# Kernel optimization log

Hardware: AMD Instinct MI355X
Metric: run time of the kernel (lower is better)

## Reference

```python
import jax, jax.numpy as jnp
import numpy as np


def conv2d(x, w, b, pad):
    # x: [B,Cin,H,W], w: [Cout,Cin,kh,kw]
    y = jax.lax.conv_general_dilated(
        x, w, window_strides=(1, 1), padding=[(pad, pad), (pad, pad)],
        dimension_numbers=('NCHW', 'OIHW', 'NCHW'))
    return y + b[None, :, None, None]


def setup_inputs() -> dict:
    key = jax.random.key(0)
    ks = jax.random.split(key, 11)
    B, C, H, W = 4, 128, 64, 64
    Cc, Hc, Wc = 256, 32, 32
    s = 0.05
    return {
        'sr_feat': jax.random.normal(ks[0], (B, C, H, W), jnp.float32),
        'context_feat': jax.random.normal(ks[1], (B, Cc, Hc, Wc), jnp.float32),
        'Wq': jax.random.normal(ks[2], (C, C, 1, 1), jnp.float32) * s,
        'bq': jax.random.normal(ks[3], (C,), jnp.float32) * s,
        'Wk': jax.random.normal(ks[4], (C, Cc, 1, 1), jnp.float32) * s,
        'bk': jax.random.normal(ks[5], (C,), jnp.float32) * s,
        'Wv': jax.random.normal(ks[6], (C, Cc, 1, 1), jnp.float32) * s,
        'bv': jax.random.normal(ks[7], (C,), jnp.float32) * s,
        'Wp': jax.random.normal(ks[8], (C, C, 3, 3), jnp.float32) * s,
        'bp': jax.random.normal(ks[9], (C,), jnp.float32) * s,
        'gamma': jax.random.normal(ks[10], (1,), jnp.float32) * s,
    }


def reference(sr_feat, context_feat, Wq, bq, Wk, bk, Wv, bv, Wp, bp, gamma):
    B, C, H, W = sr_feat.shape
    Cc = context_feat.shape[1]
    # bilinear upsample (half-pixel centers == align_corners=False)
    ctx = jax.image.resize(context_feat, (B, Cc, H, W), method='bilinear')
    q = conv2d(sr_feat, Wq, bq, 0).reshape(B, C, H * W)   # [B,C,N]
    k = conv2d(ctx, Wk, bk, 0).reshape(B, C, H * W)       # [B,C,N]
    v = conv2d(ctx, Wv, bv, 0).reshape(B, C, H * W)       # [B,C,N]
    # attn[b,n,m] = softmax_m( sum_c q[b,c,n] * k[b,c,m] )
    attn = jax.nn.softmax(jnp.einsum('bcn,bcm->bnm', q, k), axis=-1)
    # out[b,c,n] = sum_m v[b,c,m] * attn[b,n,m]
    out = jnp.einsum('bcm,bnm->bcn', v, attn).reshape(B, C, H, W)
    return sr_feat + gamma[0] * conv2d(out, Wp, bp, 1)
```

## Files before the change

### kernel.cpp

```cpp
#include <hip/hip_runtime.h>
#include <math.h>

#define NB 4
#define C  128
#define CCH 256
#define HH 64
#define WW 64
#define NN 4096
#define HC 32
#define WC 32
#define PP 66
#define LOG2E 1.44269504088896f
#define NSPLIT 4

typedef unsigned short u16;
typedef unsigned int uint32;
typedef short s16x8 __attribute__((ext_vector_type(8)));
typedef float f32x4 __attribute__((ext_vector_type(4)));
typedef float f32x16 __attribute__((ext_vector_type(16)));

__device__ __forceinline__ u16 f2bf(float f) {
    uint32 u = __float_as_uint(f);
    u += 0x7fffu + ((u >> 16) & 1u);
    return (u16)(u >> 16);
}
__device__ __forceinline__ float bf2f(u16 h) {
    return __uint_as_float((uint32)h << 16);
}

__global__ __launch_bounds__(256) void prep_all(const float* __restrict__ ctx,
                                                const float* __restrict__ sr,
                                                const float* __restrict__ Wq,
                                                const float* __restrict__ Wk,
                                                const float* __restrict__ Wv,
                                                const float* __restrict__ Wp,
                                                u16* __restrict__ ctx_t,
                                                u16* __restrict__ sr_t,
                                                u16* __restrict__ wbf,
                                                u16* __restrict__ wt,
                                                uint4* __restrict__ att_z) {
    __shared__ float smem[2 * 32 * 130];
    int blk = blockIdx.x;
    int tid = threadIdx.x;

    if (blk < 512) {
        float (*ls)[32][130] = (float(*)[32][130])smem;
        int y = blk & 63;
        int cch = (blk >> 6) & 1;
        int b = blk >> 7;
        float sy = y * 0.5f - 0.25f;
        int y0 = (int)floorf(sy);
        float wy = sy - (float)y0;
        int y0c = y0 < 0 ? 0 : y0;
        int y1c = (y0 + 1 > HC - 1) ? HC - 1 : y0 + 1;
#pragma unroll
        for (int t = 0; t < 4; t++) {
            int CI = t * 256 + tid;
            int cc = CI >> 3, xq = CI & 7;
            const float* s = ctx + (size_t)(b * CCH + cch * 128 + cc) * (HC * WC);
            float4 v0 = *(const float4*)(s + y0c * WC + xq * 4);
            float4 v1 = *(const float4*)(s + y1c * WC + xq * 4);
            ls[0][xq * 4 + 0][cc] = v0.x; ls[0][xq * 4 + 1][cc] = v0.y;
            ls[0][xq * 4 + 2][cc] = v0.z; ls[0][xq * 4 + 3][cc] = v0.w;
            ls[1][xq * 4 + 0][cc] = v1.x; ls[1][xq * 4 + 1][cc] = v1.y;
            ls[1][xq * 4 + 2][cc] = v1.z; ls[1][xq * 4 + 3][cc] = v1.w;
        }
        __syncthreads();
        int occ = tid & 127, xh = tid >> 7;
        u16* ob = ctx_t + ((size_t)b * NN + (size_t)y * 64) * CCH + cch * 128 + occ;
        float wy1 = 1.f - wy;
#pragma unroll
        for (int xi = 0; xi < 32; xi++) {
            int x = xi * 2 + xh;
            float sx = x * 0.5f - 0.25f;
            int x0 = (int)floorf(sx);
            float wx = sx - (float)x0;
            int x0c = x0 < 0 ? 0 : x0;
            int x1c = (x0 + 1 > WC - 1) ? WC - 1 : x0 + 1;
            float v00 = ls[0][x0c][occ], v01 = ls[0][x1c][occ];
            float v10 = ls[1][x0c][occ], v11 = ls[1][x1c][occ];
            float val = wy1 * ((1.f - wx) * v00 + wx * v01)
                      + wy  * ((1.f - wx) * v10 + wx * v11);
            ob[(size_t)x * CCH] = f2bf(val);
        }
    } else if (blk < 1024) {
        float* ls = smem;
        int idx = blk - 512;
        int n0 = (idx & 63) * 64;
        int ci0 = ((idx >> 6) & 1) * 64;
        int b = idx >> 7;
        const float* inb = sr + ((size_t)b * C + ci0) * NN + n0;
#pragma unroll
        for (int L = 0; L < 4; L++) {
            int fc = tid + L * 256;
            int nc = fc & 15, ci = fc >> 4;
            float4 v = *(const float4*)(inb + (size_t)ci * NN + nc * 4);
            float* d = &ls[ci * 65 + nc * 4];
            d[0] = v.x; d[1] = v.y; d[2] = v.z; d[3] = v.w;
        }
        __syncthreads();
        u16* ob = sr_t + ((size_t)b * NN + n0) * C + ci0;
#pragma unroll
        for (int j = 0; j < 16; j++) {
            int o = tid + j * 256;
            int ci = o & 63, n = o >> 6;
            ob[(size_t)n * C + ci] = f2bf(ls[ci * 65 + n]);
        }
    } else if (blk < 1920) {
        int i = (blk - 1024) * 256 + tid;
        if (i < 81920) {
            float v;
            if (i < 16384) v = Wq[i] * LOG2E;
            else if (i < 49152) v = Wk[i - 16384];
            else v = Wv[i - 49152];
            wbf[i] = f2bf(v);
        } else {
            int idx = i - 81920;
            int ciin = idx & 31;
            int co = (idx >> 5) & 127;
            int cb = (idx >> 12) & 3;
            int pos = idx >> 14;
            int ky = pos / 3, kx = pos - ky * 3;
            int ci = cb * 32 + ciin;
            wt[idx] = f2bf(Wp[((size_t)(co * C + ci) * 3 + ky) * 3 + kx]);
        }
    } else {
        int i = (blk - 1920) * 256 + tid;
        if (i < 278784) att_z[i] = make_uint4(0, 0, 0, 0);
    }
}

__global__ __launch_bounds__(256) void proj_all(const u16* __restrict__ sr_t,
                                                const u16* __restrict__ ctx_t,
                                                const u16* __restrict__ wbf,
                                                const float* __restrict__ bq,
                                                const float* __restrict__ bk,
                                                const float* __restrict__ bv,
                                                u16* __restrict__ q_t,
                                                u16* __restrict__ k_t,
                                                u16* __restrict__ v_bf) {
    __shared__ u16 xs[128 * 64];
    __shared__ u16 wsm[128 * 64];
    int z = blockIdx.z;
    int b = blockIdx.y;
    int n0 = blockIdx.x * 128;
    int Cin = (z == 0) ? C : CCH;
    const u16* xb = (z == 0 ? sr_t : ctx_t) + (size_t)b * NN * Cin;
    const u16* wb = wbf + (z == 0 ? 0 : (z == 1 ? 16384 : 49152));
    const float* bias = (z == 0) ? bq : (z == 1 ? bk : bv);
    float bsc = (z == 0) ? LOG2E : 1.0f;
    bool vmode = (z == 2);

    int tid = threadIdx.x;
    int w = tid >> 6, lane = tid & 63, l31 = lane & 31, half = lane >> 5;
    int xh = w >> 1, wh = w & 1;

    f32x16 acc[2][2];
#pragma unroll
    for (int xt = 0; xt < 2; xt++)
#pragma unroll
        for (int wt2 = 0; wt2 < 2; wt2++)
#pragma unroll
            for (int i = 0; i < 16; i++) acc[xt][wt2][i] = 0.f;

    int nchunks = Cin >> 6;
    for (int c0i = 0; c0i < nchunks; c0i++) {
        int c0 = c0i * 64;
        __syncthreads();
#pragma unroll
        for (int t = 0; t < 4; t++) {
            int CI = t * 256 + tid;
            int row = CI >> 3, sl = CI & 7;
            int lc = sl ^ (row & 7);
            __builtin_amdgcn_global_load_lds(
                (const __attribute__((address_space(1))) void*)(xb + (size_t)(n0 + row) * Cin + c0 + lc * 8),
                (__attribute__((address_space(3))) void*)&xs[(size_t)CI * 8], 16, 0, 0);
        }
#pragma unroll
        for (int t = 0; t < 4; t++) {
            int CI = t * 256 + tid;
            int co = CI >> 3, sl = CI & 7;
            int lc = sl ^ (co & 7);
            __builtin_amdgcn_global_load_lds(
                (const __attribute__((address_space(1))) void*)(wb + (size_t)co * Cin + c0 + lc * 8),
                (__attribute__((address_space(3))) void*)&wsm[(size_t)CI * 8], 16, 0, 0);
        }
        __syncthreads();
#pragma unroll
        for (int kg = 0; kg < 4; kg++) {
            int pc = ((kg * 2 + half) ^ (l31 & 7)) * 8;
            s16x8 xf[2], wf2[2];
#pragma unroll
            for (int xt = 0; xt < 2; xt++)
                xf[xt] = *(const s16x8*)&xs[(xh * 64 + xt * 32 + l31) * 64 + pc];
#pragma unroll
            for (int wt2 = 0; wt2 < 2; wt2++)
                wf2[wt2] = *(const s16x8*)&wsm[(wh * 64 + wt2 * 32 + l31) * 64 + pc];
#pragma unroll
            for (int xt = 0; xt < 2; xt++)
#pragma unroll
                for (int wt2 = 0; wt2 < 2; wt2++) {
                    if (vmode)
                        acc[xt][wt2] = __builtin_amdgcn_mfma_f32_32x32x16_bf16(wf2[wt2], xf[xt], acc[xt][wt2], 0, 0, 0);
                    else
                        acc[xt][wt2] = __builtin_amdgcn_mfma_f32_32x32x16_bf16(xf[xt], wf2[wt2], acc[xt][wt2], 0, 0, 0);
                }
        }
    }

    if (!vmode) {
        u16* ot = (z == 0 ? q_t : k_t) + (size_t)b * NN * C;
        float bv2[2];
#pragma unroll
        for (int wt2 = 0; wt2 < 2; wt2++) bv2[wt2] = bias[wh * 64 + wt2 * 32 + l31] * bsc;
#pragma unroll
        for (int xt = 0; xt < 2; xt++)
#pragma unroll
            for (int r = 0; r < 16; r++) {
                int n = n0 + xh * 64 + xt * 32 + (r & 3) + 8 * (r >> 2) + 4 * half;
#pragma unroll
                for (int wt2 = 0; wt2 < 2; wt2++)
                    ot[(size_t)n * C + wh * 64 + wt2 * 32 + l31] = f2bf(acc[xt][wt2][r] + bv2[wt2]);
            }
    } else {
        u16* ov = v_bf + (size_t)b * C * NN;
#pragma unroll
        for (int wt2 = 0; wt2 < 2; wt2++)
#pragma unroll
            for (int r = 0; r < 16; r++) {
                int co = wh * 64 + wt2 * 32 + (r & 3) + 8 * (r >> 2) + 4 * half;
                float bvv = bias[co];
#pragma unroll
                for (int xt = 0; xt < 2; xt++) {
                    int n = n0 + xh * 64 + xt * 32 + l31;
                    ov[(size_t)co * NN + n] = f2bf(acc[xt][wt2][r] + bvv);
                }
            }
    }
}

__global__ __launch_bounds__(256) void flash_mfma(const u16* __restrict__ qt_p,
                                                  const u16* __restrict__ kt_p,
                                                  const u16* __restrict__ vt_p,
                                                  u16* __restrict__ part,
                                                  float* __restrict__ lpart) {
    __shared__ u16 ks[64 * 128];
    __shared__ u16 vs[128 * 64];

    int ib = blockIdx.x;
    int b = (ib & 7) >> 1;
    int rest = ((ib >> 3) << 1) | (ib & 1);
    int qtile = rest >> 2;
    int split = rest & 3;
    int n0 = qtile * 128;
    int tid = threadIdx.x;
    int w = tid >> 6, lane = tid & 63, l31 = lane & 31, half = lane >> 5;

    const u16* qtb = qt_p + (size_t)b * NN * C;
    const u16* ktb = kt_p + (size_t)b * NN * C;
    const u16* vtb = vt_p + (size_t)b * C * NN;

    auto stageK = [&](int m0) {
#pragma unroll
        for (int t = 0; t < 4; t++) {
            int CI = (w * 4 + t) * 64 + lane;
            int r = CI >> 4;
            int lc = (CI & 15) ^ (r & 15);
            __builtin_amdgcn_global_load_lds(
                (const __attribute__((address_space(1))) void*)(ktb + (size_t)(m0 + r) * C + lc * 8),
                (__attribute__((address_space(3))) void*)&ks[(w * 4 + t) * 512], 16, 0, 0);
        }
    };
    auto stageV = [&](int m0) {
#pragma unroll
        for (int t = 0; t < 4; t++) {
            int CI = (w * 4 + t) * 64 + lane;
            int c = CI >> 3;
            int lc = (CI & 7) ^ (c & 7);
            __builtin_amdgcn_global_load_lds(
                (const __attribute__((address_space(1))) void*)(vtb + (size_t)c * NN + m0 + lc * 8),
                (__attribute__((address_space(3))) void*)&vs[(w * 4 + t) * 512], 16, 0, 0);
        }
    };

    int qrow = n0 + w * 32 + l31;
    s16x8 qf[8];
#pragma unroll
    for (int kg = 0; kg < 8; kg++)
        qf[kg] = *(const s16x8*)(qtb + (size_t)qrow * C + kg * 16 + half * 8);

    int m_base = split * 1024;
    stageK(m_base);
    __syncthreads();

    f32x16 oacc[4];
#pragma unroll
    for (int mt = 0; mt < 4; mt++)
#pragma unroll
        for (int i = 0; i < 16; i++) oacc[mt][i] = 0.f;
    float lsum = 0.f;

    for (int it = 0; it < 16; it++) {
        int m0 = m_base + it * 64;
        stageV(m0);

        f32x16 st[2];
#pragma unroll
        for (int kmt = 0; kmt < 2; kmt++)
#pragma unroll
            for (int i = 0; i < 16; i++) st[kmt][i] = 0.f;
#pragma unroll
        for (int kg = 0; kg < 8; kg++) {
            int pc = ((kg * 2 + half) ^ (l31 & 15)) * 8;
#pragma unroll
            for (int kmt = 0; kmt < 2; kmt++) {
                s16x8 kf = *(const s16x8*)&ks[(kmt * 32 + l31) * 128 + pc];
                st[kmt] = __builtin_amdgcn_mfma_f32_32x32x16_bf16(kf, qf[kg], st[kmt], 0, 0, 0);
            }
        }
        __syncthreads();
        if (it < 15) stageK(m0 + 64);

#pragma unroll
        for (int kmt = 0; kmt < 2; kmt++) {
            float e[16];
            float ls = 0.f;
#pragma unroll
            for (int r = 0; r < 16; r++) { e[r] = exp2f(st[kmt][r]); ls += e[r]; }
            lsum += ls;
            uint32 A[4], B4[4];
#pragma unroll
            for (int g = 0; g < 4; g++) {
                A[g]  = __builtin_amdgcn_perm(__float_as_uint(e[4 * g + 1]), __float_as_uint(e[4 * g + 0]), 0x07060302u);
                B4[g] = __builtin_amdgcn_perm(__float_as_uint(e[4 * g + 3]), __float_as_uint(e[4 * g + 2]), 0x07060302u);
            }
#pragma unroll
            for (int s = 0; s < 2; s++) {
                uint32 sendA = half ? A[2 * s] : A[2 * s + 1];
                uint32 sendB = half ? B4[2 * s] : B4[2 * s + 1];
                uint32 rA = __shfl_xor(sendA, 32);
                uint32 rB = __shfl_xor(sendB, 32);
                uint32 oA = half ? A[2 * s + 1] : A[2 * s];
                uint32 oB = half ? B4[2 * s + 1] : B4[2 * s];
                union { uint32 u[4]; s16x8 v; } pu;
                pu.u[0] = half ? rA : oA;
                pu.u[1] = half ? rB : oB;
                pu.u[2] = half ? oA : rA;
                pu.u[3] = half ? oB : rB;
                s16x8 pf = pu.v;
                int kgp = kmt * 2 + s;
                int pcv = ((kgp * 2 + half) ^ (l31 & 7)) * 8;
#pragma unroll
                for (int mt = 0; mt < 4; mt++) {
                    s16x8 vf = *(const s16x8*)&vs[(mt * 32 + l31) * 64 + pcv];
                    oacc[mt] = __builtin_amdgcn_mfma_f32_32x32x16_bf16(vf, pf, oacc[mt], 0, 0, 0);
                }
            }
        }
        __syncthreads();
    }

    float lt = lsum + __shfl_xor(lsum, 32);
    if (half == 0) lpart[(size_t)split * NB * NN + (size_t)b * NN + qrow] = lt;
    u16* pb = part + ((size_t)split * NB + b) * (size_t)C * NN;
#pragma unroll
    for (int mt = 0; mt < 4; mt++)
#pragma unroll
        for (int r = 0; r < 16; r++) {
            int c = mt * 32 + (r & 3) + 8 * (r >> 2) + 4 * half;
            pb[(size_t)c * NN + n0 + w * 32 + l31] = f2bf(oacc[mt][r]);
        }
}

__global__ __launch_bounds__(256) void flash_combine(const u16* __restrict__ part,
                                                     const float* __restrict__ lpart,
                                                     u16* __restrict__ att_t) {
    __shared__ u16 ts[128 * 66];
    __shared__ float linv[64];
    int b = blockIdx.y;
    int nt = blockIdx.x;
    int n0 = nt * 64;
    int tid = threadIdx.x;
    if (tid < 64) {
        float s = 0.f;
#pragma unroll
        for (int sp = 0; sp < NSPLIT; sp++)
            s += lpart[(size_t)sp * NB * NN + (size_t)b * NN + n0 + tid];
        linv[tid] = 1.0f / s;
    }
    __syncthreads();
#pragma unroll
    for (int j = 0; j < 32; j++) {
        int e = tid + j * 256;
        int n = e & 63, c = e >> 6;
        float o = 0.f;
#pragma unroll
        for (int sp = 0; sp < NSPLIT; sp++)
            o += bf2f(part[((size_t)sp * NB + b) * (size_t)C * NN + (size_t)c * NN + n0 + n]);
        ts[c * 66 + n] = f2bf(o * linv[n]);
    }
    __syncthreads();
    u16* ob = att_t + ((size_t)b * PP * PP + (size_t)(nt + 1) * PP + 1) * C;
#pragma unroll
    for (int j = 0; j < 32; j++) {
        int o = tid + j * 256;
        int c = o & 127, n = o >> 7;
        ob[(size_t)n * C + c] = ts[c * 66 + n];
    }
}

__global__ __launch_bounds__(256) void conv3x3_mfma(const u16* __restrict__ att_t,
                                                    const u16* __restrict__ wt,
                                                    const float* __restrict__ bp,
                                                    const float* __restrict__ sr,
                                                    const float* __restrict__ gamma,
                                                    float* __restrict__ out) {
    __shared__ u16 in_s[2][4 * 102 * 8];
    int ib = blockIdx.x;
    int b = (ib & 7) >> 1;
    int rr = ((ib >> 3) << 1) | (ib & 1);
    int y = rr >> 1;
    int x0 = (rr & 1) * 32;
    int tid = threadIdx.x;
    int w = tid >> 6, lane = tid & 63, l = tid & 15, quad = (tid >> 4) & 3;
    const u16* ab = att_t + (size_t)b * (PP * PP * C);

    auto stage = [&](int cib, int bufi) {
        u16* base = &in_s[bufi][w * 102 * 8];
        const u16* gsrc = ab + cib * 32 + w * 8;
#pragma unroll
        for (int t = 0; t < 2; t++) {
            int idx = t * 64 + lane;
            int r = idx / 34, xp = idx - r * 34;
            if (t == 0 || lane < 38)
                __builtin_amdgcn_global_load_lds(
                    (const __attribute__((address_space(1))) void*)(gsrc + (size_t)((y + r) * PP + x0 + xp) * C),
                    (__attribute__((address_space(3))) void*)(base + (size_t)t * 64 * 8), 16, 0, 0);
        }
    };

    f32x4 accr[2][2];
#pragma unroll
    for (int cf = 0; cf < 2; cf++)
#pragma unroll
        for (int nf = 0; nf < 2; nf++) accr[cf][nf] = (f32x4){0.f, 0.f, 0.f, 0.f};
    int cow = w * 32;

    stage(0, 0);
    __syncthreads();
#pragma unroll
    for (int cib = 0; cib < 4; cib++) {
        if (cib < 3) stage(cib + 1, (cib + 1) & 1);
        s16x8 wf[9][2];
#pragma unroll
        for (int pos = 0; pos < 9; pos++)
#pragma unroll
            for (int cf = 0; cf < 2; cf++)
                wf[pos][cf] = *(const s16x8*)&wt[((size_t)(pos * 4 + cib) * C + cow + cf * 16 + l) * 32 + quad * 8];
        const u16* bufc = &in_s[cib & 1][0];
#pragma unroll
        for (int ky = 0; ky < 3; ky++)
#pragma unroll
            for (int kx = 0; kx < 3; kx++) {
                int pos = ky * 3 + kx;
#pragma unroll
                for (int nf = 0; nf < 2; nf++) {
                    s16x8 inf = *(const s16x8*)&bufc[(quad * 102 + ky * 34 + nf * 16 + l + kx) * 8];
                    accr[0][nf] = __builtin_amdgcn_mfma_f32_16x16x32_bf16(wf[pos][0], inf, accr[0][nf], 0, 0, 0);
                    accr[1][nf] = __builtin_amdgcn_mfma_f32_16x16x32_bf16(wf[pos][1], inf, accr[1][nf], 0, 0, 0);
                }
            }
        __syncthreads();
    }

    float g = gamma[0];
    float* ob = out + (size_t)b * C * NN;
    const float* sb = sr + (size_t)b * C * NN;
#pragma unroll
    for (int cf = 0; cf < 2; cf++)
#pragma unroll
        for (int r = 0; r < 4; r++) {
            int co = cow + cf * 16 + quad * 4 + r;
            float bias = bp[co];
#pragma unroll
            for (int nf = 0; nf < 2; nf++) {
                size_t oo = (size_t)co * NN + y * 64 + x0 + nf * 16 + l;
                ob[oo] = sb[oo] + g * (accr[cf][nf][r] + bias);
            }
        }
}

extern "C" void kernel_launch(void* const* d_in, const int* in_sizes, int n_in,
                              void* d_out, int out_size, void* d_ws, size_t ws_size,
                              hipStream_t stream) {
    const float* sr    = (const float*)d_in[0];
    const float* ctx   = (const float*)d_in[1];
    const float* Wq    = (const float*)d_in[2];
    const float* bq    = (const float*)d_in[3];
    const float* Wk    = (const float*)d_in[4];
    const float* bk    = (const float*)d_in[5];
    const float* Wv    = (const float*)d_in[6];
    const float* bv    = (const float*)d_in[7];
    const float* Wp    = (const float*)d_in[8];
    const float* bp    = (const float*)d_in[9];
    const float* gamma = (const float*)d_in[10];
    float* out = (float*)d_out;

    char* wsb = (char*)d_ws;
    u16*   att_t  = (u16*)wsb;
    u16*   part   = (u16*)(wsb + (5u << 20));
    float* lpart  = (float*)(wsb + (21u << 20));
    u16*   ctx_t  = (u16*)(wsb + (22u << 20));
    u16*   sr_t   = (u16*)(wsb + (30u << 20));
    u16*   q_t    = (u16*)(wsb + (34u << 20));
    u16*   k_t    = (u16*)(wsb + (38u << 20));
    u16*   v_bf   = (u16*)(wsb + (42u << 20));
    u16*   wt     = (u16*)(wsb + (46u << 20));
    u16*   w_bf   = (u16*)(wsb + (46u << 20) + (512u << 10));

    prep_all<<<dim3(3009), 256, 0, stream>>>(ctx, sr, Wq, Wk, Wv, Wp,
                                             ctx_t, sr_t, w_bf, wt,
                                             (uint4*)att_t);
    proj_all<<<dim3(32, NB, 3), 256, 0, stream>>>(sr_t, ctx_t, w_bf, bq, bk, bv,
                                                  q_t, k_t, v_bf);
    flash_mfma<<<dim3(512), 256, 0, stream>>>(q_t, k_t, v_bf, part, lpart);
    flash_combine<<<dim3(64, NB), 256, 0, stream>>>(part, lpart, att_t);
    conv3x3_mfma<<<dim3(512), 256, 0, stream>>>(att_t, wt, bp, sr, gamma, out);
}
```

Measured before the change: 168.4 us.

## Double-buffer K/V tiles in flash attention and use hardware exp2

Allocates two LDS buffers each for the K and V tiles so the next 64-key tile is prefetched while the current one is consumed. This removes the mid-iteration barrier between the QK and PV phases. The score computation is also split per 32-key half, so each half's softmax and PV MMA follow right after its own QK MMA, which lowers register pressure. exp2f is replaced by the raw hardware exp2 builtin. LDS use doubles to 64KB per block, which may reduce occupancy.

```diff
diff --git a/kernel.cpp b/kernel.cpp
--- a/kernel.cpp
+++ b/kernel.cpp
@@ -18,6 +18,12 @@
 typedef short s16x8 __attribute__((ext_vector_type(8)));
 typedef float f32x4 __attribute__((ext_vector_type(4)));
 typedef float f32x16 __attribute__((ext_vector_type(16)));
+
+#if __has_builtin(__builtin_amdgcn_exp2f)
+#define EXP2(x) __builtin_amdgcn_exp2f(x)
+#else
+#define EXP2(x) __expf((x) * 0.69314718056f)
+#endif
 
 __device__ __forceinline__ u16 f2bf(float f) {
     uint32 u = __float_as_uint(f);
@@ -244,8 +250,8 @@
                                                   const u16* __restrict__ vt_p,
                                                   u16* __restrict__ part,
                                                   float* __restrict__ lpart) {
-    __shared__ u16 ks[64 * 128];
-    __shared__ u16 vs[128 * 64];
+    __shared__ u16 ks[2][64 * 128];
+    __shared__ u16 vs[2][128 * 64];
 
     int ib = blockIdx.x;
     int b = (ib & 7) >> 1;
@@ -260,7 +266,7 @@
     const u16* ktb = kt_p + (size_t)b * NN * C;
     const u16* vtb = vt_p + (size_t)b * C * NN;
 
-    auto stageK = [&](int m0) {
+    auto stageK = [&](int buf, int m0) {
 #pragma unroll
         for (int t = 0; t < 4; t++) {
             int CI = (w * 4 + t) * 64 + lane;
@@ -268,10 +274,10 @@
             int lc = (CI & 15) ^ (r & 15);
             __builtin_amdgcn_global_load_lds(
                 (const __attribute__((address_space(1))) void*)(ktb + (size_t)(m0 + r) * C + lc * 8),
-                (__attribute__((address_space(3))) void*)&ks[(w * 4 + t) * 512], 16, 0, 0);
+                (__attribute__((address_space(3))) void*)&ks[buf][(w * 4 + t) * 512], 16, 0, 0);
         }
     };
-    auto stageV = [&](int m0) {
+    auto stageV = [&](int buf, int m0) {
 #pragma unroll
         for (int t = 0; t < 4; t++) {
             int CI = (w * 4 + t) * 64 + lane;
@@ -279,7 +285,7 @@
             int lc = (CI & 7) ^ (c & 7);
             __builtin_amdgcn_global_load_lds(
                 (const __attribute__((address_space(1))) void*)(vtb + (size_t)c * NN + m0 + lc * 8),
-                (__attribute__((address_space(3))) void*)&vs[(w * 4 + t) * 512], 16, 0, 0);
+                (__attribute__((address_space(3))) void*)&vs[buf][(w * 4 + t) * 512], 16, 0, 0);
         }
     };
 
@@ -290,7 +296,8 @@
         qf[kg] = *(const s16x8*)(qtb + (size_t)qrow * C + kg * 16 + half * 8);
 
     int m_base = split * 1024;
-    stageK(m_base);
+    stageK(0, m_base);
+    stageV(0, m_base);
     __syncthreads();
 
     f32x16 oacc[4];
@@ -301,38 +308,36 @@
     float lsum = 0.f;
 
     for (int it = 0; it < 16; it++) {
+        int buf = it & 1;
         int m0 = m_base + it * 64;
-        stageV(m0);
-
-        f32x16 st[2];
-#pragma unroll
-        for (int kmt = 0; kmt < 2; kmt++)
-#pragma unroll
-            for (int i = 0; i < 16; i++) st[kmt][i] = 0.f;
-#pragma unroll
-        for (int kg = 0; kg < 8; kg++) {
-            int pc = ((kg * 2 + half) ^ (l31 & 15)) * 8;
-#pragma unroll
-            for (int kmt = 0; kmt < 2; kmt++) {
-                s16x8 kf = *(const s16x8*)&ks[(kmt * 32 + l31) * 128 + pc];
-                st[kmt] = __builtin_amdgcn_mfma_f32_32x32x16_bf16(kf, qf[kg], st[kmt], 0, 0, 0);
-            }
-        }
-        __syncthreads();
-        if (it < 15) stageK(m0 + 64);
+        if (it < 15) {
+            stageK(buf ^ 1, m0 + 64);
+            stageV(buf ^ 1, m0 + 64);
+        }
+        const u16* ksb = &ks[buf][0];
+        const u16* vsb = &vs[buf][0];
 
 #pragma unroll
         for (int kmt = 0; kmt < 2; kmt++) {
-            float e[16];
-            float ls = 0.f;
-#pragma unroll
-            for (int r = 0; r < 16; r++) { e[r] = exp2f(st[kmt][r]); ls += e[r]; }
-            lsum += ls;
+            f32x16 st;
+#pragma unroll
+            for (int i = 0; i < 16; i++) st[i] = 0.f;
+#pragma unroll
+            for (int kg = 0; kg < 8; kg++) {
+                int pc = ((kg * 2 + half) ^ (l31 & 15)) * 8;
+                s16x8 kf = *(const s16x8*)&ksb[(kmt * 32 + l31) * 128 + pc];
+                st = __builtin_amdgcn_mfma_f32_32x32x16_bf16(kf, qf[kg], st, 0, 0, 0);
+            }
             uint32 A[4], B4[4];
 #pragma unroll
-            for (int g = 0; g < 4; g++) {
-                A[g]  = __builtin_amdgcn_perm(__float_as_uint(e[4 * g + 1]), __float_as_uint(e[4 * g + 0]), 0x07060302u);
-                B4[g] = __builtin_amdgcn_perm(__float_as_uint(e[4 * g + 3]), __float_as_uint(e[4 * g + 2]), 0x07060302u);
+            for (int rg = 0; rg < 4; rg++) {
+                float e0 = EXP2(st[rg * 4 + 0]);
+                float e1 = EXP2(st[rg * 4 + 1]);
+                float e2 = EXP2(st[rg * 4 + 2]);
+                float e3 = EXP2(st[rg * 4 + 3]);
+                lsum += (e0 + e1) + (e2 + e3);
+                A[rg]  = __builtin_amdgcn_perm(__float_as_uint(e1), __float_as_uint(e0), 0x07060302u);
+                B4[rg] = __builtin_amdgcn_perm(__float_as_uint(e3), __float_as_uint(e2), 0x07060302u);
             }
 #pragma unroll
             for (int s = 0; s < 2; s++) {
@@ -352,7 +357,7 @@
                 int pcv = ((kgp * 2 + half) ^ (l31 & 7)) * 8;
 #pragma unroll
                 for (int mt = 0; mt < 4; mt++) {
-                    s16x8 vf = *(const s16x8*)&vs[(mt * 32 + l31) * 64 + pcv];
+                    s16x8 vf = *(const s16x8*)&vsb[(mt * 32 + l31) * 64 + pcv];
                     oacc[mt] = __builtin_amdgcn_mfma_f32_32x32x16_bf16(vf, pf, oacc[mt], 0, 0, 0);
                 }
             }
```

Result: faster. 161.9 us (-3.8%).
